# Kernel tuning notes

Measured on AMD Instinct MI355X. Metric: run time of the kernel, lower is better.

The kernel has to match this reference:

```python
import jax, jax.numpy as jnp
import numpy as np

B, TD, TE = 32, 64, 64     # batch, decoder len, encoder len
V, D, H = 32000, 512, 512  # vocab, embed dim, hidden


def setup_inputs() -> dict:
    key = jax.random.key(0)
    ks = jax.random.split(key, 11)
    return {
        "xs": jax.random.randint(ks[0], (B, TD), 0, V),
        "hs": jax.random.normal(ks[1], (B, TE, H), jnp.float32),
        "h0": jax.random.normal(ks[2], (B, H), jnp.float32) * 0.1,
        "c0": jax.random.normal(ks[3], (B, H), jnp.float32) * 0.1,
        "embed_W": jax.random.normal(ks[4], (V, D), jnp.float32) * 0.01,
        "W_ih": jax.random.normal(ks[5], (4 * H, D), jnp.float32) / np.sqrt(D).astype(np.float32),
        "W_hh": jax.random.normal(ks[6], (4 * H, H), jnp.float32) / np.sqrt(H).astype(np.float32),
        "b_ih": jnp.zeros((4 * H,), jnp.float32),
        "b_hh": jnp.zeros((4 * H,), jnp.float32),
        "aff_W": jax.random.normal(ks[7], (V, 2 * H), jnp.float32) / np.sqrt(H).astype(np.float32),
        "aff_b": jnp.zeros((V,), jnp.float32),
    }


def _lstm(emb, h0, c0, W_ih, W_hh, b):
    # emb: [B, T, D]; PyTorch gate order i, f, g, o
    xp = jnp.einsum('btd,gd->btg', emb, W_ih) + b  # [B, T, 4H], input proj precomputed

    def step(carry, x_t):
        h, c = carry
        gates = x_t + h @ W_hh.T  # [B, 4H]
        i, f, g, o = jnp.split(gates, 4, axis=-1)
        c = jax.nn.sigmoid(f) * c + jax.nn.sigmoid(i) * jnp.tanh(g)
        h = jax.nn.sigmoid(o) * jnp.tanh(c)
        return (h, c), h

    (hT, cT), hseq = jax.lax.scan(step, (h0, c0), jnp.swapaxes(xp, 0, 1))
    return jnp.swapaxes(hseq, 0, 1), hT, cT  # [B, T, H]


def reference(xs, hs, h0, c0, embed_W, W_ih, W_hh, b_ih, b_hh, aff_W, aff_b):
    emb = embed_W[xs]  # [B, TD, D]
    out, hT, cT = _lstm(emb, h0, c0, W_ih, W_hh, b_ih + b_hh)  # out: [B, TD, H]
    # scores s = bmm(hs, out^T): [B, TE, TD]; softmax over encoder axis (dim=1)
    s = jnp.einsum('beh,bth->bet', hs, out)
    attention_weight = jax.nn.softmax(s, axis=1)
    # context: vectorized form of the original per-timestep loop
    c = jnp.einsum('bet,beh->bth', attention_weight, hs)  # [B, TD, H]
    feat = jnp.concatenate([out, c], axis=-1)  # [B, TD, 2H]
    logits = jnp.einsum('btf,vf->btv', feat, aff_W) + aff_b  # [B, TD, V]
    return logits, hT, cT, attention_weight
```

## Files before the change

kernel.cpp:

```cpp
#include <hip/hip_runtime.h>


typedef unsigned short u16;
typedef unsigned int u32;
typedef __bf16 bf16x8 __attribute__((ext_vector_type(8)));
typedef float f32x4 __attribute__((ext_vector_type(4)));
typedef u32 u32x4 __attribute__((ext_vector_type(4)));

__device__ __forceinline__ float bf2f(u16 u){ u32 x = ((u32)u)<<16; return __builtin_bit_cast(float, x); }
__device__ __forceinline__ u16 f2bf(float f){ u32 x = __builtin_bit_cast(u32, f); x += 0x7FFFu + ((x>>16)&1u); return (u16)(x>>16); }
__device__ __forceinline__ u32 pk2(float a, float b){ return (u32)f2bf(a) | ((u32)f2bf(b)<<16); }
__device__ __forceinline__ u32x4 pk8(const float* p){
  f32x4 lo = *(const f32x4*)p, hi = *(const f32x4*)(p+4);
  u32x4 r; r[0]=pk2(lo[0],lo[1]); r[1]=pk2(lo[2],lo[3]); r[2]=pk2(hi[0],hi[1]); r[3]=pk2(hi[2],hi[3]);
  return r;
}

__device__ __forceinline__ f32x4 mfma16(u32x4 a, u32x4 b, f32x4 c){
  return __builtin_amdgcn_mfma_f32_16x16x32_bf16(
      __builtin_bit_cast(bf16x8, a), __builtin_bit_cast(bf16x8, b), c, 0, 0, 0);
}

__device__ __forceinline__ void gld16(const void* g, void* l){
  __builtin_amdgcn_global_load_lds(
      (__attribute__((address_space(1))) void*)(void*)g,
      (__attribute__((address_space(3))) void*)l, 16, 0, 0);
}

__device__ __forceinline__ void st_cc(u32* p, u32 v){
  asm volatile("global_store_dword %0, %1, off sc0 sc1" :: "v"(p), "v"(v) : "memory");
}
__device__ __forceinline__ u32x4 ld_cc4(const u32* p){
  u32x4 r;
  asm volatile("global_load_dwordx4 %0, %1, off sc0 sc1" : "=v"(r) : "v"(p) : "memory");
  return r;
}

__device__ __forceinline__ float sigm(float x){ x = fminf(fmaxf(x,-30.f),30.f); return 1.f/(1.f+__expf(-x)); }
__device__ __forceinline__ float tanh_ap(float x){ float xc = fminf(fmaxf(x,-15.f),15.f); float e = __expf(-2.f*xc); return (1.f-e)/(1.f+e); }

__global__ void k_init(const float* __restrict__ h0, u16* __restrict__ hbuf1, u32* __restrict__ flags){
  int i = blockIdx.x*256 + threadIdx.x;
  hbuf1[i] = f2bf(h0[i]);
  if (i < 32) flags[i] = 0u;
}

__global__ __launch_bounds__(256) void k_xp(const int* __restrict__ xs,
    const float* __restrict__ embW, const float* __restrict__ Wih,
    const float* __restrict__ bih, const float* __restrict__ bhh,
    u16* __restrict__ xpb)
{
  __shared__ u16 sm[16384];
  u16* As = sm; u16* Bs = sm + 8192;
  const int tid = threadIdx.x;
  const int m0 = blockIdx.x*128, n0 = blockIdx.y*128;
  const int wave = tid>>6, lane = tid&63, quad = lane>>4, lr = lane&15;
  const int wm = wave>>1, wn = wave&1;
  const int rbase = tid>>3, cb = (tid&7)*8;
  int tok[4];
  #pragma unroll
  for (int i=0;i<4;i++) tok[i] = xs[m0 + i*32 + rbase];
  f32x4 acc[4][4];
  #pragma unroll
  for (int i=0;i<4;i++)
    #pragma unroll
    for (int j=0;j<4;j++) acc[i][j] = (f32x4){0.f,0.f,0.f,0.f};

  for (int kb=0; kb<512; kb+=64){
    #pragma unroll
    for (int i=0;i<4;i++)
      *(u32x4*)(As + i*2048 + tid*8) = pk8(embW + (long)tok[i]*512 + kb + cb);
    #pragma unroll
    for (int i=0;i<4;i++)
      *(u32x4*)(Bs + i*2048 + tid*8) = pk8(Wih + (long)(n0 + i*32 + rbase)*512 + kb + cb);
    __syncthreads();
    #pragma unroll
    for (int k0=0;k0<64;k0+=32){
      u32x4 bf[4];
      #pragma unroll
      for (int j=0;j<4;j++) bf[j] = *(const u32x4*)(Bs + (wn*64 + j*16 + lr)*64 + k0 + quad*8);
      #pragma unroll
      for (int i=0;i<4;i++){
        u32x4 af = *(const u32x4*)(As + (wm*64 + i*16 + lr)*64 + k0 + quad*8);
        #pragma unroll
        for (int j=0;j<4;j++) acc[i][j] = mfma16(af, bf[j], acc[i][j]);
      }
    }
    __syncthreads();
  }
  float bias[4];
  #pragma unroll
  for (int j=0;j<4;j++){ int col = n0 + wn*64 + j*16 + lr; bias[j] = bih[col] + bhh[col]; }
  #pragma unroll
  for (int i=0;i<4;i++)
    #pragma unroll
    for (int j=0;j<4;j++){
      int row = m0 + wm*64 + i*16 + quad*4;
      int col = n0 + wn*64 + j*16 + lr;
      #pragma unroll
      for (int r=0;r<4;r++) xpb[(long)(row+r)*2048 + col] = f2bf(acc[i][j][r] + bias[j]);
    }
}

__global__ __launch_bounds__(256) void k_lstm(const u16* __restrict__ xpb,
    const float* __restrict__ c0, const float* __restrict__ Whh,
    u16* __restrict__ feat, u16* __restrict__ hbuf, u32* __restrict__ flags,
    float* __restrict__ outH, float* __restrict__ outC)
{
  __shared__ u16 hS[16384];
  __shared__ float gacc[4][32][16];
  const int tid = threadIdx.x, w = blockIdx.x;
  const int wave = tid>>6, lane = tid&63, quad = lane>>4, lr = lane&15;
  const int cbase = w*16;

  u32x4 bfrag[16];
  const float* wrow = Whh + (long)(wave*512 + cbase + lr)*512;
  #pragma unroll
  for (int kit=0;kit<16;kit++) bfrag[kit] = pk8(wrow + kit*32 + quad*8);

  const int bb0 = tid>>3;
  const int cc0 = (tid*2)&15;
  float cst[2];
  cst[0] = c0[bb0*512 + cbase + cc0];
  cst[1] = c0[bb0*512 + cbase + cc0 + 1];

  u32* hb32 = (u32*)hbuf;

  u32 xv[4];
  {
    const u16* xp0 = xpb + (long)(bb0*64)*2048 + cbase + cc0;
    #pragma unroll
    for (int q=0;q<4;q++) xv[q] = *(const u32*)(xp0 + q*512);
  }

  for (int t=0;t<64;t++){
    if (t>0){
      if (wave==0){
        for(;;){
          u32 f = __hip_atomic_load(flags + (lane&31), __ATOMIC_RELAXED, __HIP_MEMORY_SCOPE_AGENT);
          if (__all((int)(f >= (u32)t))) break;
        }
      }
      __syncthreads();
    }
    const u32* src = hb32 + ((t+1)&1)*8192;
    u32x4 hreg[8];
    #pragma unroll
    for (int k=0;k<8;k++) hreg[k] = ld_cc4(src + k*1024 + tid*4);
    asm volatile("s_waitcnt vmcnt(0)" ::: "memory");
    __builtin_amdgcn_sched_barrier(0);
    #pragma unroll
    for (int k=0;k<8;k++){
      int row  = k*4 + (tid>>6);
      int colb = (tid&63)*16;
      *(u32x4*)((char*)hS + row*1024 + (colb ^ ((row&7)<<4))) = hreg[k];
    }
    __syncthreads();

    f32x4 acc0 = {0.f,0.f,0.f,0.f}, acc1 = {0.f,0.f,0.f,0.f};
    #pragma unroll
    for (int kit=0;kit<16;kit++){
      int colb = (kit*64 + quad*16) ^ ((lr&7)<<4);
      u32x4 a0 = *(const u32x4*)((char*)hS + lr*1024 + colb);
      u32x4 a1 = *(const u32x4*)((char*)hS + (16+lr)*1024 + colb);
      acc0 = mfma16(a0, bfrag[kit], acc0);
      acc1 = mfma16(a1, bfrag[kit], acc1);
    }
    #pragma unroll
    for (int r=0;r<4;r++){
      gacc[wave][quad*4+r][lr]    = acc0[r];
      gacc[wave][16+quad*4+r][lr] = acc1[r];
    }
    __syncthreads();

    float hv[2];
    #pragma unroll
    for (int j=0;j<2;j++){
      float gi = gacc[0][bb0][cc0+j] + bf2f((u16)(xv[0] >> (16*j)));
      float gf = gacc[1][bb0][cc0+j] + bf2f((u16)(xv[1] >> (16*j)));
      float gg = gacc[2][bb0][cc0+j] + bf2f((u16)(xv[2] >> (16*j)));
      float go = gacc[3][bb0][cc0+j] + bf2f((u16)(xv[3] >> (16*j)));
      float cn = sigm(gf)*cst[j] + sigm(gi)*tanh_ap(gg);
      cst[j] = cn;
      hv[j] = sigm(go)*tanh_ap(cn);
    }
    *(u32*)(feat + (long)(bb0*64 + t)*1024 + cbase + cc0) = pk2(hv[0],hv[1]);

    if (t < 63){
      st_cc(hb32 + (t&1)*8192 + bb0*256 + (cbase>>1) + (tid&7), pk2(hv[0],hv[1]));
      asm volatile("s_waitcnt vmcnt(0)" ::: "memory");
      __syncthreads();
      if (tid==0)
        __hip_atomic_store(flags + w, (u32)(t+1), __ATOMIC_RELAXED, __HIP_MEMORY_SCOPE_AGENT);
      const u16* xp0 = xpb + (long)(bb0*64 + t+1)*2048 + cbase + cc0;
      #pragma unroll
      for (int q=0;q<4;q++) xv[q] = *(const u32*)(xp0 + q*512);
    } else {
      *(float2*)(outH + bb0*512 + cbase + cc0) = make_float2(hv[0], hv[1]);
      *(float2*)(outC + bb0*512 + cbase + cc0) = make_float2(cst[0], cst[1]);
    }
  }
}

__global__ __launch_bounds__(256) void k_attn(const float* __restrict__ hs,
    u16* __restrict__ feat, float* __restrict__ attnOut)
{
  __shared__ u16 stg[16384];
  __shared__ float sS[4096];
  __shared__ u16 aT[4096];
  __shared__ float red[8][64];
  const int tid = threadIdx.x, b = blockIdx.x;
  const int wave = tid>>6, lane = tid&63, quad = lane>>4, lr = lane&15;
  const float* hsb = hs + (long)b*32768;

  f32x4 sacc[4];
  #pragma unroll
  for (int j=0;j<4;j++) sacc[j] = (f32x4){0.f,0.f,0.f,0.f};
  for (int kk=0; kk<2; kk++){
    int row = tid>>2, cc0 = (tid&3)*64;
    #pragma unroll
    for (int c8=0; c8<8; c8++)
      *(u32x4*)(stg + row*256 + cc0 + c8*8) = pk8(hsb + (long)row*512 + kk*256 + cc0 + c8*8);
    __syncthreads();
    for (int kit=0; kit<8; kit++){
      u32x4 af = *(const u32x4*)(stg + (wave*16 + lr)*256 + kit*32 + quad*8);
      #pragma unroll
      for (int j=0;j<4;j++){
        u32x4 bfv = *(const u32x4*)(feat + (long)(b*64 + j*16 + lr)*1024 + kk*256 + kit*32 + quad*8);
        sacc[j] = mfma16(af, bfv, sacc[j]);
      }
    }
    __syncthreads();
  }
  #pragma unroll
  for (int j=0;j<4;j++)
    #pragma unroll
    for (int r=0;r<4;r++)
      sS[(wave*16 + quad*4 + r)*64 + j*16 + lr] = sacc[j][r];
  __syncthreads();

  {
    int t = tid&63, qtr = tid>>6;
    float m = -1e30f;
    for (int e=qtr*16; e<qtr*16+16; e++) m = fmaxf(m, sS[e*64+t]);
    red[qtr][t] = m;
    __syncthreads();
    m = fmaxf(fmaxf(red[0][t],red[1][t]), fmaxf(red[2][t],red[3][t]));
    float sum = 0.f;
    for (int e=qtr*16; e<qtr*16+16; e++) sum += __expf(sS[e*64+t]-m);
    red[4+qtr][t] = sum;
    __syncthreads();
    float inv = 1.f/(red[4][t]+red[5][t]+red[6][t]+red[7][t]);
    for (int e=qtr*16; e<qtr*16+16; e++){
      float wgt = __expf(sS[e*64+t]-m)*inv;
      aT[t*64+e] = f2bf(wgt);
      attnOut[b*4096 + e*64 + t] = wgt;
    }
  }
  __syncthreads();

  for (int hh=0; hh<2; hh++){
    #pragma unroll
    for (int it=0; it<8; it++){
      int g = tid*8 + it, e = g>>5, hb = g&31;
      const float* p = hsb + (long)e*512 + hh*256 + hb*8;
      f32x4 lo = *(const f32x4*)p, hi = *(const f32x4*)(p+4);
      stg[(hb*8+0)*64 + e] = f2bf(lo[0]);
      stg[(hb*8+1)*64 + e] = f2bf(lo[1]);
      stg[(hb*8+2)*64 + e] = f2bf(lo[2]);
      stg[(hb*8+3)*64 + e] = f2bf(lo[3]);
      stg[(hb*8+4)*64 + e] = f2bf(hi[0]);
      stg[(hb*8+5)*64 + e] = f2bf(hi[1]);
      stg[(hb*8+6)*64 + e] = f2bf(hi[2]);
      stg[(hb*8+7)*64 + e] = f2bf(hi[3]);
    }
    __syncthreads();
    u32x4 a0 = *(const u32x4*)(aT + (wave*16+lr)*64 + quad*8);
    u32x4 a1 = *(const u32x4*)(aT + (wave*16+lr)*64 + 32 + quad*8);
    for (int hn=0; hn<16; hn++){
      f32x4 c = {0.f,0.f,0.f,0.f};
      u32x4 b0 = *(const u32x4*)(stg + (hn*16+lr)*64 + quad*8);
      u32x4 b1 = *(const u32x4*)(stg + (hn*16+lr)*64 + 32 + quad*8);
      c = mfma16(a0, b0, c);
      c = mfma16(a1, b1, c);
      int hcol = hh*256 + hn*16 + lr;
      #pragma unroll
      for (int r=0;r<4;r++){
        int t = wave*16 + quad*4 + r;
        feat[(long)(b*64 + t)*1024 + 512 + hcol] = f2bf(c[r]);
      }
    }
    __syncthreads();
  }
}

__global__ __launch_bounds__(256) void k_logits(const u16* __restrict__ feat,
    const float* __restrict__ affW, const float* __restrict__ affb, float* __restrict__ outL)
{
  __shared__ u16 sm[16384];
  u16* As = sm; u16* Bs = sm + 8192;
  const int tid = threadIdx.x;
  const int m0 = blockIdx.x*128, n0 = blockIdx.y*128;
  const int wave = tid>>6, lane = tid&63, quad = lane>>4, lr = lane&15;
  const int wm = wave>>1, wn = wave&1;
  const int rbase = tid>>3, cb = (tid&7)*8;
  f32x4 acc[4][4];
  #pragma unroll
  for (int i=0;i<4;i++)
    #pragma unroll
    for (int j=0;j<4;j++) acc[i][j] = (f32x4){0.f,0.f,0.f,0.f};

  for (int kb=0; kb<1024; kb+=64){
    #pragma unroll
    for (int i=0;i<4;i++)
      gld16(feat + (long)(m0 + i*32 + rbase)*1024 + kb + cb, As + i*2048 + tid*8);
    #pragma unroll
    for (int i=0;i<4;i++)
      *(u32x4*)(Bs + i*2048 + tid*8) = pk8(affW + (long)(n0 + i*32 + rbase)*1024 + kb + cb);
    __syncthreads();
    #pragma unroll
    for (int k0=0;k0<64;k0+=32){
      u32x4 bf[4];
      #pragma unroll
      for (int j=0;j<4;j++) bf[j] = *(const u32x4*)(Bs + (wn*64 + j*16 + lr)*64 + k0 + quad*8);
      #pragma unroll
      for (int i=0;i<4;i++){
        u32x4 af = *(const u32x4*)(As + (wm*64 + i*16 + lr)*64 + k0 + quad*8);
        #pragma unroll
        for (int j=0;j<4;j++) acc[i][j] = mfma16(af, bf[j], acc[i][j]);
      }
    }
    __syncthreads();
  }
  float bias[4];
  #pragma unroll
  for (int j=0;j<4;j++) bias[j] = affb[n0 + wn*64 + j*16 + lr];
  #pragma unroll
  for (int i=0;i<4;i++)
    #pragma unroll
    for (int j=0;j<4;j++){
      int row = m0 + wm*64 + i*16 + quad*4;
      int col = n0 + wn*64 + j*16 + lr;
      #pragma unroll
      for (int r=0;r<4;r++) outL[(long)(row+r)*32000 + col] = acc[i][j][r] + bias[j];
    }
}

extern "C" void kernel_launch(void* const* d_in, const int* in_sizes, int n_in,
                              void* d_out, int out_size, void* d_ws, size_t ws_size,
                              hipStream_t stream) {
  const int*   xs   = (const int*)d_in[0];
  const float* hs   = (const float*)d_in[1];
  const float* h0   = (const float*)d_in[2];
  const float* c0   = (const float*)d_in[3];
  const float* embW = (const float*)d_in[4];
  const float* Wih  = (const float*)d_in[5];
  const float* Whh  = (const float*)d_in[6];
  const float* bih  = (const float*)d_in[7];
  const float* bhh  = (const float*)d_in[8];
  const float* affW = (const float*)d_in[9];
  const float* affb = (const float*)d_in[10];
  float* out = (float*)d_out;

  char* ws = (char*)d_ws;
  u16* xpb   = (u16*)ws;
  u16* feat  = (u16*)(ws + 8388608);
  u16* hbuf  = (u16*)(ws + 8388608 + 4194304);
  u32* flags = (u32*)(ws + 8388608 + 4194304 + 65536);

  float* outHT  = out + 65536000;
  float* outCT  = out + 65552384;
  float* outAtt = out + 65568768;

  k_init<<<64, 256, 0, stream>>>(h0, hbuf + 16384, flags);
  k_xp<<<dim3(16,16), 256, 0, stream>>>(xs, embW, Wih, bih, bhh, xpb);
  k_lstm<<<32, 256, 0, stream>>>(xpb, c0, Whh, feat, hbuf, flags, outHT, outCT);
  k_attn<<<32, 256, 0, stream>>>(hs, feat, outAtt);
  k_logits<<<dim3(16,250), 256, 0, stream>>>(feat, affW, affb, out);
}
```

Baseline: 883.3 us.

## Pre-convert affine weights to bf16 in idle LSTM blocks and swizzle logits grid

The LSTM kernel is launched with extra blocks that convert the fp32 output projection weights to bf16 in workspace while the 32 recurrent blocks run the sequential scan, hiding the conversion behind latency-bound work. A new logits GEMM then loads the bf16 weights directly through LDS DMA instead of converting fp32 per tile, and remaps block indices so blocks sharing weight tiles run close together for L2 reuse. It relies on the workspace being large enough and falls back to the old path otherwise. The extra blocks could contend for bandwidth with the LSTM or disturb its flag-based cross-block sync if residency is affected.

```diff
diff --git a/kernel.cpp b/kernel.cpp
--- a/kernel.cpp
+++ b/kernel.cpp
@@ -105,11 +105,22 @@
 __global__ __launch_bounds__(256) void k_lstm(const u16* __restrict__ xpb,
     const float* __restrict__ c0, const float* __restrict__ Whh,
     u16* __restrict__ feat, u16* __restrict__ hbuf, u32* __restrict__ flags,
-    float* __restrict__ outH, float* __restrict__ outC)
+    float* __restrict__ outH, float* __restrict__ outC,
+    const float* __restrict__ affW, u16* __restrict__ affWb)
 {
   __shared__ u16 hS[16384];
   __shared__ float gacc[4][32][16];
   const int tid = threadIdx.x, w = blockIdx.x;
+
+  if (w >= 32){
+    const long N = 32768000L;
+    long i = ((long)(w - 32)*256 + tid)*8;
+    const long stride = (long)(gridDim.x - 32)*256*8;
+    for (; i < N; i += stride)
+      *(u32x4*)(affWb + i) = pk8(affW + i);
+    return;
+  }
+
   const int wave = tid>>6, lane = tid&63, quad = lane>>4, lr = lane&15;
   const int cbase = w*16;
 
@@ -292,6 +303,60 @@
     }
     __syncthreads();
   }
+}
+
+__global__ __launch_bounds__(256) void k_logits_bw(const u16* __restrict__ feat,
+    const u16* __restrict__ affWb, const float* __restrict__ affb, float* __restrict__ outL)
+{
+  __shared__ u16 sm[16384];
+  u16* As = sm; u16* Bs = sm + 8192;
+  const int tid = threadIdx.x;
+  const int flat = blockIdx.x;
+  const int logical = (flat & 7)*500 + (flat >> 3);
+  const int m0 = (logical & 15)*128, n0 = (logical >> 4)*128;
+  const int wave = tid>>6, lane = tid&63, quad = lane>>4, lr = lane&15;
+  const int wm = wave>>1, wn = wave&1;
+  const int rbase = tid>>3, cb = (tid&7)*8;
+  f32x4 acc[4][4];
+  #pragma unroll
+  for (int i=0;i<4;i++)
+    #pragma unroll
+    for (int j=0;j<4;j++) acc[i][j] = (f32x4){0.f,0.f,0.f,0.f};
+
+  for (int kb=0; kb<1024; kb+=64){
+    #pragma unroll
+    for (int i=0;i<4;i++)
+      gld16(feat + (long)(m0 + i*32 + rbase)*1024 + kb + cb, As + i*2048 + tid*8);
+    #pragma unroll
+    for (int i=0;i<4;i++)
+      gld16(affWb + (long)(n0 + i*32 + rbase)*1024 + kb + cb, Bs + i*2048 + tid*8);
+    __syncthreads();
+    #pragma unroll
+    for (int k0=0;k0<64;k0+=32){
+      u32x4 bf[4];
+      #pragma unroll
+      for (int j=0;j<4;j++) bf[j] = *(const u32x4*)(Bs + (wn*64 + j*16 + lr)*64 + k0 + quad*8);
+      #pragma unroll
+      for (int i=0;i<4;i++){
+        u32x4 af = *(const u32x4*)(As + (wm*64 + i*16 + lr)*64 + k0 + quad*8);
+        #pragma unroll
+        for (int j=0;j<4;j++) acc[i][j] = mfma16(af, bf[j], acc[i][j]);
+      }
+    }
+    __syncthreads();
+  }
+  float bias[4];
+  #pragma unroll
+  for (int j=0;j<4;j++) bias[j] = affb[n0 + wn*64 + j*16 + lr];
+  #pragma unroll
+  for (int i=0;i<4;i++)
+    #pragma unroll
+    for (int j=0;j<4;j++){
+      int row = m0 + wm*64 + i*16 + quad*4;
+      int col = n0 + wn*64 + j*16 + lr;
+      #pragma unroll
+      for (int r=0;r<4;r++) outL[(long)(row+r)*32000 + col] = acc[i][j][r] + bias[j];
+    }
 }
 
 __global__ __launch_bounds__(256) void k_logits(const u16* __restrict__ feat,
@@ -367,6 +432,8 @@
   u16* feat  = (u16*)(ws + 8388608);
   u16* hbuf  = (u16*)(ws + 8388608 + 4194304);
   u32* flags = (u32*)(ws + 8388608 + 4194304 + 65536);
+  u16* affWb = (u16*)(ws + 12648576);
+  const bool useBf = ws_size >= (size_t)(12648576) + 65536000;
 
   float* outHT  = out + 65536000;
   float* outCT  = out + 65552384;
@@ -374,7 +441,10 @@
 
   k_init<<<64, 256, 0, stream>>>(h0, hbuf + 16384, flags);
   k_xp<<<dim3(16,16), 256, 0, stream>>>(xs, embW, Wih, bih, bhh, xpb);
-  k_lstm<<<32, 256, 0, stream>>>(xpb, c0, Whh, feat, hbuf, flags, outHT, outCT);
+  k_lstm<<<useBf ? 256 : 32, 256, 0, stream>>>(xpb, c0, Whh, feat, hbuf, flags, outHT, outCT, affW, affWb);
   k_attn<<<32, 256, 0, stream>>>(hs, feat, outAtt);
-  k_logits<<<dim3(16,250), 256, 0, stream>>>(feat, affW, affb, out);
-}
+  if (useBf)
+    k_logits_bw<<<4000, 256, 0, stream>>>(feat, affWb, affb, out);
+  else
+    k_logits<<<dim3(16,250), 256, 0, stream>>>(feat, affW, affb, out);
+}
```

Result: faster. 767.6 us (-13.1%).
